# Kernel optimization log

Hardware: AMD Instinct MI355X
Metric: run time of the kernel (lower is better)

Reference implementation:

```python
import jax, jax.numpy as jnp
import numpy as np
from math import factorial as _f

E = 131072          # number of neighbour pairs (edges)
N_ATOMS = 8192
NUM_RADIAL = 16
L_BASIS = 3         # basis_max_degree -> 16 SH components
L_MOMENT = 4        # moment_max_degree -> 25 components
CUTOFF = 5.0

# ---------- Clebsch-Gordan coefficients (real spherical-harmonic basis) ----------

def _cg(j1, m1, j2, m2, j3, m3):
    if m1 + m2 != m3 or not (abs(j1 - j2) <= j3 <= j1 + j2):
        return 0.0
    pre = ((2 * j3 + 1) * _f(j3 + j1 - j2) * _f(j3 - j1 + j2) * _f(j1 + j2 - j3) / _f(j1 + j2 + j3 + 1)) ** 0.5
    pre *= (_f(j3 + m3) * _f(j3 - m3) * _f(j1 - m1) * _f(j1 + m1) * _f(j2 - m2) * _f(j2 + m2)) ** 0.5
    s = 0.0
    for k in range(max(0, j2 - j3 - m1, j1 - j3 + m2), min(j1 + j2 - j3, j1 - m1, j2 + m2) + 1):
        s += (-1.0) ** k / (_f(k) * _f(j1 + j2 - j3 - k) * _f(j1 - m1 - k) * _f(j2 + m2 - k) * _f(j3 - j2 + m1 + k) * _f(j3 - j1 - m2 + k))
    return pre * s

def _u(l):
    # complex -> real SH change of basis; rows index real m, cols complex m'
    U = np.zeros((2 * l + 1, 2 * l + 1), dtype=np.complex128)
    U[l, l] = 1.0
    s2 = 2.0 ** -0.5
    for m in range(1, l + 1):
        U[l + m, l + m] = (-1) ** m * s2
        U[l + m, l - m] = s2
        U[l - m, l - m] = 1j * s2
        U[l - m, l + m] = -1j * (-1) ** m * s2
    return U

def _real_cg(l1, l2, l3):
    C = np.zeros((2 * l1 + 1, 2 * l2 + 1, 2 * l3 + 1), dtype=np.complex128)
    for a in range(2 * l1 + 1):
        for b in range(2 * l2 + 1):
            for c in range(2 * l3 + 1):
                C[a, b, c] = _cg(l1, a - l1, l2, b - l2, l3, c - l3)
    M = np.einsum('ia,jb,kc,abc->ijk', _u(l1), _u(l2), _u(l3).conj(), C)
    R, I = M.real, M.imag  # coefficients are purely real or purely imaginary per path
    out = R if np.abs(R).sum() >= np.abs(I).sum() else I
    return out.astype(np.float32)

def _paths(lin, lout):
    return [(l1, l2, l3)
            for l1 in range(lin + 1) for l2 in range(lin + 1)
            for l3 in range(abs(l1 - l2), min(l1 + l2, lout) + 1)]

PATHS1 = _paths(L_BASIS, L_MOMENT)   # 40 paths
PATHS2 = _paths(L_MOMENT, L_MOMENT)  # 67 paths
CG1 = [jnp.asarray(_real_cg(*p)) for p in PATHS1]
CG2 = [jnp.asarray(_real_cg(*p)) for p in PATHS2]

# ---------- spherical harmonics up to l=3 (orthonormal real SH) ----------

def _sph_harm(u):
    x, y, z = u[:, 0], u[:, 1], u[:, 2]
    x2, y2, z2 = x * x, y * y, z * z
    sh = [
        jnp.full_like(x, 0.28209479177387814),
        0.4886025119029199 * y, 0.4886025119029199 * z, 0.4886025119029199 * x,
        1.0925484305920792 * x * y, 1.0925484305920792 * y * z,
        0.31539156525252005 * (3.0 * z2 - 1.0),
        1.0925484305920792 * x * z, 0.5462742152960396 * (x2 - y2),
        0.5900435899266435 * y * (3.0 * x2 - y2), 2.890611442640554 * x * y * z,
        0.4570457994644658 * y * (5.0 * z2 - 1.0), 0.3731763325901154 * z * (5.0 * z2 - 3.0),
        0.4570457994644658 * x * (5.0 * z2 - 1.0), 1.445305721320277 * z * (x2 - y2),
        0.5900435899266435 * x * (x2 - 3.0 * y2),
    ]
    return jnp.stack(sh, axis=-1)  # (E, 16)

def _basis(disp):
    r = jnp.linalg.norm(disp, axis=-1)                         # (E,)
    u = disp / jnp.maximum(r, 1e-9)[:, None]
    x = r / CUTOFF
    # sinc radial basis: sinc((k+1) * r / cutoff), k = 0..NUM_RADIAL-1
    rb = jnp.sinc(x[:, None] * jnp.arange(1, NUM_RADIAL + 1, dtype=disp.dtype))  # (E, K)
    # smooth (bump) cutoff, nan-safe under grad
    x2 = jnp.where(x < 1.0, x * x, 0.0)
    cut = jnp.where(x < 1.0, jnp.exp(1.0 - 1.0 / (1.0 - x2)), 0.0)
    sh = _sph_harm(u)                                          # (E, 16)
    return (cut[:, None] * sh)[:, :, None] * rb[:, None, :]    # (E, 16, K)

def _fused_tensor(y, w, paths, cgs):
    # y: (E, (Lin+1)^2, F); one learnable weight per CG path per feature
    dim_out = (L_MOMENT + 1) ** 2
    out = jnp.zeros((y.shape[0], dim_out, y.shape[-1]), dtype=y.dtype)
    for p, ((l1, l2, l3), C) in enumerate(zip(paths, cgs)):
        y1 = y[:, l1 * l1:(l1 + 1) ** 2, :]
        y2 = y[:, l2 * l2:(l2 + 1) ** 2, :]
        z = jnp.einsum('eif,ejf,ijk->ekf', y1, y2, C.astype(y.dtype))
        out = out.at[:, l3 * l3:(l3 + 1) ** 2, :].add(w[p] * z)
    return out


def setup_inputs() -> dict:
    key = jax.random.key(0)
    k1, k2, k3, k4, k5 = jax.random.split(key, 5)
    return {
        "atomic_numbers": jax.random.randint(k1, (N_ATOMS,), 0, 100, dtype=jnp.int32),
        "neighbour_displacements": jax.random.normal(k2, (E, 3), dtype=jnp.float32) * 2.0,
        "neighbour_indices": jax.random.randint(k3, (E, 2), 0, N_ATOMS),
        "tp_weights1": jax.random.normal(k4, (len(PATHS1), NUM_RADIAL), dtype=jnp.float32) * 0.2,
        "tp_weights2": jax.random.normal(k5, (len(PATHS2), NUM_RADIAL), dtype=jnp.float32) * 0.2,
    }


def reference(atomic_numbers, neighbour_displacements, neighbour_indices, tp_weights1, tp_weights2):
    y = _basis(neighbour_displacements)                 # (E, 16, F)
    y = _fused_tensor(y, tp_weights1, PATHS1, CG1)      # (E, 25, F)  moment 2
    y = _fused_tensor(y, tp_weights2, PATHS2, CG2)      # (E, 25, F)  moment 3
    return y
```

## Files before the change

kernel.cpp:

```cpp
#include <hip/hip_runtime.h>
#include <utility>

typedef unsigned int  u32;
typedef unsigned short u16;


struct CEnt { int i, j, k; double c; };
struct PathTab { int n; int s; CEnt e[400]; };
struct cxd { double re, im; };
struct URow { int n; int col[2]; cxd v[2]; };
struct MTab { double M[9][9][9]; };

constexpr double FT[14] = {1.,1.,2.,6.,24.,120.,720.,5040.,40320.,362880.,
                           3628800.,39916800.,479001600.,6227020800.};

constexpr double cabs_(double x){ return x < 0 ? -x : x; }

constexpr double csqrt_(double x){
  if (x <= 0.) return 0.;
  double g = 1.;
  while (g*g < x) g *= 2.;
  for (int it = 0; it < 50; ++it) g = 0.5*(g + x/g);
  return g;
}

constexpr double cg_(int j1,int m1,int j2,int m2,int j3,int m3){
  if (m1 + m2 != m3) return 0.;
  int dj = j1 - j2; if (dj < 0) dj = -dj;
  if (j3 < dj || j3 > j1 + j2) return 0.;
  double preA = (double)(2*j3+1)*FT[j3+j1-j2]*FT[j3-j1+j2]*FT[j1+j2-j3]/FT[j1+j2+j3+1];
  double preB = FT[j3+m3]*FT[j3-m3]*FT[j1-m1]*FT[j1+m1]*FT[j2-m2]*FT[j2+m2];
  double pre = csqrt_(preA)*csqrt_(preB);
  int kmin = 0;
  if (j2-j3-m1 > kmin) kmin = j2-j3-m1;
  if (j1-j3+m2 > kmin) kmin = j1-j3+m2;
  int kmax = j1+j2-j3;
  if (j1-m1 < kmax) kmax = j1-m1;
  if (j2+m2 < kmax) kmax = j2+m2;
  double s = 0.;
  for (int k = kmin; k <= kmax; ++k){
    double d = FT[k]*FT[j1+j2-j3-k]*FT[j1-m1-k]*FT[j2+m2-k]*FT[j3-j2+m1+k]*FT[j3-j1-m2+k];
    s += ((k & 1) ? -1.0 : 1.0)/d;
  }
  return pre*s;
}

constexpr URow urow_(int l, int r){
  URow R{};
  const double s2 = 0.7071067811865476;
  int m = r - l;
  if (m == 0){ R.n = 1; R.col[0] = l; R.v[0] = {1., 0.}; }
  else if (m > 0){
    R.n = 2;
    R.col[0] = l + m; R.v[0] = { (m & 1) ? -s2 : s2, 0. };
    R.col[1] = l - m; R.v[1] = { s2, 0. };
  } else {
    int mm = -m;
    R.n = 2;
    R.col[0] = l - mm; R.v[0] = { 0., s2 };
    R.col[1] = l + mm; R.v[1] = { 0., (mm & 1) ? s2 : -s2 };
  }
  return R;
}

constexpr cxd cmul_(cxd a, cxd b){ return { a.re*b.re - a.im*b.im, a.re*b.im + a.im*b.re }; }

constexpr MTab buildM(int l1, int l2, int l3){
  const int n1 = 2*l1+1, n2 = 2*l2+1, n3 = 2*l3+1;
  double cgd[9][9][9] = {};
  for (int a = 0; a < n1; ++a)
    for (int b = 0; b < n2; ++b)
      for (int c = 0; c < n3; ++c)
        cgd[a][b][c] = cg_(l1, a-l1, l2, b-l2, l3, c-l3);

  double MR[9][9][9] = {}; double MI[9][9][9] = {};
  double sR = 0., sI = 0.;
  for (int i = 0; i < n1; ++i){
    URow u1 = urow_(l1, i);
    for (int j = 0; j < n2; ++j){
      URow u2 = urow_(l2, j);
      for (int k = 0; k < n3; ++k){
        URow u3 = urow_(l3, k);
        double mre = 0., mim = 0.;
        for (int a = 0; a < u1.n; ++a)
          for (int b = 0; b < u2.n; ++b)
            for (int c = 0; c < u3.n; ++c){
              double cv = cgd[u1.col[a]][u2.col[b]][u3.col[c]];
              if (cv != 0.){
                cxd t = cmul_(u1.v[a], u2.v[b]);
                cxd u3c = { u3.v[c].re, -u3.v[c].im };
                t = cmul_(t, u3c);
                mre += t.re*cv; mim += t.im*cv;
              }
            }
        MR[i][j][k] = mre; MI[i][j][k] = mim;
        sR += cabs_(mre); sI += cabs_(mim);
      }
    }
  }
  const bool useR = (sR >= sI);
  MTab out{};
  for (int i = 0; i < n1; ++i)
    for (int j = 0; j < n2; ++j)
      for (int k = 0; k < n3; ++k)
        out.M[i][j][k] = useR ? MR[i][j][k] : MI[i][j][k];
  return out;
}

constexpr PathTab buildDiag(int l, int l3){
  MTab A = buildM(l, l, l3);
  PathTab P{}; P.n = 0; P.s = 1;
  const int n = 2*l+1, n3 = 2*l3+1;
  for (int i = 0; i < n; ++i)
    for (int j = i; j < n; ++j)
      for (int k = 0; k < n3; ++k){
        double v = A.M[i][j][k];
        if (j > i) v += A.M[j][i][k];
        if (cabs_(v) > 1e-12){
          if (P.n >= 400) { P.n = -1; return P; }
          P.e[P.n].i = i; P.e[P.n].j = j; P.e[P.n].k = k; P.e[P.n].c = v; P.n++;
        }
      }
  return P;
}

constexpr PathTab buildPair(int l1, int l2, int l3){
  MTab A = buildM(l1, l2, l3);
  MTab B = buildM(l2, l1, l3);
  const int n1 = 2*l1+1, n2 = 2*l2+1, n3 = 2*l3+1;
  bool okp = true, okm = true;
  for (int i = 0; i < n1; ++i)
    for (int j = 0; j < n2; ++j)
      for (int k = 0; k < n3; ++k){
        double a = A.M[i][j][k], b = B.M[j][i][k];
        if (cabs_(b - a) > 1e-9) okp = false;
        if (cabs_(b + a) > 1e-9) okm = false;
      }
  PathTab P{}; P.n = 0; P.s = okp ? 1 : (okm ? -1 : 0);
  if (P.s == 0) return P;
  for (int i = 0; i < n1; ++i)
    for (int j = 0; j < n2; ++j)
      for (int k = 0; k < n3; ++k){
        double v = A.M[i][j][k];
        if (cabs_(v) > 1e-12){
          if (P.n >= 400) { P.n = -1; return P; }
          P.e[P.n].i = i; P.e[P.n].j = j; P.e[P.n].k = k; P.e[P.n].c = v; P.n++;
        }
      }
  return P;
}

constexpr PathTab buildSingleTab(int l1, int l2, int l3){
  MTab A = buildM(l1, l2, l3);
  const int n1 = 2*l1+1, n2 = 2*l2+1, n3 = 2*l3+1;
  PathTab P{}; P.n = 0; P.s = 1;
  for (int i = 0; i < n1; ++i)
    for (int j = 0; j < n2; ++j)
      for (int k = 0; k < n3; ++k){
        double v = A.M[i][j][k];
        if (cabs_(v) > 1e-12){
          if (P.n >= 400) { P.n = -1; return P; }
          P.e[P.n].i = i; P.e[P.n].j = j; P.e[P.n].k = k; P.e[P.n].c = v; P.n++;
        }
      }
  return P;
}

template<int L,int L3>          struct TD_ { static constexpr PathTab t = buildDiag(L, L3); };
template<int L1,int L2,int L3>  struct TP_ { static constexpr PathTab t = buildPair(L1, L2, L3); };
template<int L1,int L2,int L3>  struct TS_ { static constexpr PathTab t = buildSingleTab(L1, L2, L3); };

constexpr int pidx(int lin, int lout, int a, int b, int c){
  int p = 0;
  for (int l1 = 0; l1 <= lin; ++l1)
    for (int l2 = 0; l2 <= lin; ++l2){
      int lo = l1 > l2 ? l1 - l2 : l2 - l1;
      int hi = (l1 + l2 < lout) ? l1 + l2 : lout;
      for (int l3 = lo; l3 <= hi; ++l3){
        if (l1 == a && l2 == b && l3 == c) return p;
        ++p;
      }
    }
  return -1;
}

#define G1LIST(X) \
  X(0, 0,0,0) X(1, 1,1,0) X(2, 1,1,1) X(3, 1,1,2) \
  X(4, 2,2,0) X(5, 2,2,1) X(6, 2,2,2) X(7, 2,2,3) X(8, 2,2,4) \
  X(9, 3,3,0) X(10,3,3,1) X(11,3,3,2) X(12,3,3,3) X(13,3,3,4) \
  X(14,0,1,1) X(15,0,2,2) X(16,0,3,3) \
  X(17,1,2,1) X(18,1,2,2) X(19,1,2,3) \
  X(20,1,3,2) X(21,1,3,3) X(22,1,3,4) \
  X(23,2,3,1) X(24,2,3,2) X(25,2,3,3) X(26,2,3,4)

struct Grp { int l1, l2, l3; };
#define G1ITEM(i,a,b,c) {a,b,c},
constexpr Grp G1A[27] = { G1LIST(G1ITEM) };
#undef G1ITEM

struct SlotTab { int base[28]; int s[27]; int total; };
constexpr SlotTab buildSlots(){
  SlotTab T{}; int b = 0;
  for (int i = 0; i < 27; ++i){
    int l1 = G1A[i].l1, l2 = G1A[i].l2, l3 = G1A[i].l3;
    int s = (l1 == l2) ? 1 : buildPair(l1, l2, l3).s;
    T.s[i] = s;
    T.base[i] = b;
    int w = 2*l3 + 1;
    b += (l1 != l2 && s == 0) ? 2*w : w;
  }
  T.base[27] = b; T.total = b;
  return T;
}
constexpr SlotTab ST1 = buildSlots();
constexpr int NS1v = ST1.total;


template<class TT,int L1,int L2,int BASE,int... S>
__device__ __forceinline__ void accS_(const float* __restrict__ y,
                                      float* __restrict__ o,
                                      std::integer_sequence<int, S...>){
  (( o[BASE + TT::t.e[S].k] +=
       (float)TT::t.e[S].c
       * (y[L1*L1 + TT::t.e[S].i] * y[L2*L2 + TT::t.e[S].j]) ), ...);
}
template<class TT,int L1,int L2,int BASE>
__device__ __forceinline__ void accS(const float* __restrict__ y,
                                     float* __restrict__ o){
  accS_<TT,L1,L2,BASE>(y, o, std::make_integer_sequence<int, TT::t.n>{});
}

template<int L3,int BASE,int... K>
__device__ __forceinline__ void zadds_(float* __restrict__ z,
                                       const float* __restrict__ Se, float w,
                                       std::integer_sequence<int, K...>){
  (( z[L3*L3 + K] = fmaf(w, Se[BASE + K], z[L3*L3 + K]) ), ...);
}
template<int L3,int BASE>
__device__ __forceinline__ void zadds(float* __restrict__ z,
                                      const float* __restrict__ Se, float w){
  zadds_<L3,BASE>(z, Se, w, std::make_integer_sequence<int, 2*L3+1>{});
}

template<class TT,int L1,int L2,int L3,int... S>
__device__ __forceinline__ void aps_(const float* __restrict__ y,
                                     float* __restrict__ o, float we,
                                     std::integer_sequence<int, S...>){
  (( o[L3*L3 + TT::t.e[S].k] +=
       (float)TT::t.e[S].c
       * (we * (y[L1*L1 + TT::t.e[S].i] * y[L2*L2 + TT::t.e[S].j])) ), ...);
}
template<class TT,int L1,int L2,int L3>
__device__ __forceinline__ void apply_tabs_(const float* __restrict__ y,
                                            float* __restrict__ o, float we){
  aps_<TT,L1,L2,L3>(y, o, we, std::make_integer_sequence<int, TT::t.n>{});
}

#define G2LIST(X) \
  X(0,0,0) X(1,1,0) X(1,1,1) X(1,1,2) \
  X(2,2,0) X(2,2,1) X(2,2,2) X(2,2,3) X(2,2,4) \
  X(3,3,0) X(3,3,1) X(3,3,2) X(3,3,3) X(3,3,4) \
  X(4,4,0) X(4,4,1) X(4,4,2) X(4,4,3) X(4,4,4) \
  X(0,1,1) X(0,2,2) X(0,3,3) X(0,4,4) \
  X(1,2,1) X(1,2,2) X(1,2,3) X(1,3,2) X(1,3,3) X(1,3,4) X(1,4,3) X(1,4,4) \
  X(2,3,1) X(2,3,2) X(2,3,3) X(2,3,4) X(2,4,2) X(2,4,3) X(2,4,4) \
  X(3,4,1) X(3,4,2) X(3,4,3) X(3,4,4)

static __device__ __forceinline__ void zbuild_s(float* __restrict__ z,
                                                const float* __restrict__ Se,
                                                const float* __restrict__ w1s,
                                                int f){
#define GB(gi,a,b,c) { \
    if constexpr (a == b) { \
      constexpr int pA_ = pidx(3,4,a,a,c); \
      zadds<c, ST1.base[gi]>(z, Se, w1s[pA_*16 + f]); \
    } else if constexpr (ST1.s[gi] != 0) { \
      constexpr int pA_ = pidx(3,4,a,b,c), pB_ = pidx(3,4,b,a,c); \
      const float we = fmaf((float)ST1.s[gi], w1s[pB_*16 + f], w1s[pA_*16 + f]); \
      zadds<c, ST1.base[gi]>(z, Se, we); \
    } else { \
      constexpr int pA_ = pidx(3,4,a,b,c), pB_ = pidx(3,4,b,a,c); \
      zadds<c, ST1.base[gi]>(z, Se, w1s[pA_*16 + f]); \
      zadds<c, ST1.base[gi] + 2*c + 1>(z, Se, w1s[pB_*16 + f]); \
    } }
  G1LIST(GB)
#undef GB
}

static __device__ __forceinline__ void stage2_s(const float* __restrict__ z,
                                                float* __restrict__ o,
                                                const float* __restrict__ w2s,
                                                int f){
#define G2(a,b,c) { \
    if constexpr (a == b) { \
      constexpr int p_ = pidx(4,4,a,a,c); \
      apply_tabs_<TD_<a,c>, a, b, c>(z, o, w2s[p_*16 + f]); \
    } else if constexpr (TP_<a,b,c>::t.s != 0) { \
      constexpr int pA_ = pidx(4,4,a,b,c), pB_ = pidx(4,4,b,a,c); \
      const float we = fmaf((float)TP_<a,b,c>::t.s, w2s[pB_*16 + f], w2s[pA_*16 + f]); \
      apply_tabs_<TP_<a,b,c>, a, b, c>(z, o, we); \
    } else { \
      constexpr int pA_ = pidx(4,4,a,b,c), pB_ = pidx(4,4,b,a,c); \
      apply_tabs_<TS_<a,b,c>, a, b, c>(z, o, w2s[pA_*16 + f]); \
      apply_tabs_<TS_<b,a,c>, b, a, c>(z, o, w2s[pB_*16 + f]); \
    } }
  G2LIST(G2)
#undef G2
}


__global__ __launch_bounds__(64) void acmd_kernelA(
    const float* __restrict__ disp,
    float* __restrict__ Sg, int E)
{
  __shared__ float tl[64 * NS1v];

  const int lt = threadIdx.x;
  const int e  = blockIdx.x*64 + lt;

  float Sout[NS1v];
#pragma unroll
  for (int k = 0; k < NS1v; ++k) Sout[k] = 0.f;

  if (e < E){
    const float dx = disp[3*e+0], dy = disp[3*e+1], dz = disp[3*e+2];
    const float r  = sqrtf(dx*dx + dy*dy + dz*dz);
    const float x  = r * (1.0f/5.0f);
    const float inv = 1.0f / fmaxf(r, 1e-9f);
    const float ux = dx*inv, uy = dy*inv, uz = dz*inv;
    const float cut = (x < 1.0f) ? expf(1.0f - 1.0f/(1.0f - x*x)) : 0.0f;

    const float sx2 = ux*ux, sy2 = uy*uy, sz2 = uz*uz;
    float s_[16];
    s_[0]  = 0.28209479177387814f;
    s_[1]  = 0.4886025119029199f*uy;
    s_[2]  = 0.4886025119029199f*uz;
    s_[3]  = 0.4886025119029199f*ux;
    s_[4]  = 1.0925484305920792f*ux*uy;
    s_[5]  = 1.0925484305920792f*uy*uz;
    s_[6]  = 0.31539156525252005f*(3.0f*sz2 - 1.0f);
    s_[7]  = 1.0925484305920792f*ux*uz;
    s_[8]  = 0.5462742152960396f*(sx2 - sy2);
    s_[9]  = 0.5900435899266435f*uy*(3.0f*sx2 - sy2);
    s_[10] = 2.890611442640554f*ux*uy*uz;
    s_[11] = 0.4570457994644658f*uy*(5.0f*sz2 - 1.0f);
    s_[12] = 0.3731763325901154f*uz*(5.0f*sz2 - 3.0f);
    s_[13] = 0.4570457994644658f*ux*(5.0f*sz2 - 1.0f);
    s_[14] = 1.445305721320277f*uz*(sx2 - sy2);
    s_[15] = 0.5900435899266435f*ux*(sx2 - 3.0f*sy2);
#pragma unroll
    for (int i = 0; i < 16; ++i) s_[i] *= cut;

#define GA(gi,a,b,c) { \
      if constexpr (a == b) accS<TD_<a,c>, a, b, ST1.base[gi]>(s_, Sout); \
      else if constexpr (ST1.s[gi] != 0) accS<TP_<a,b,c>, a, b, ST1.base[gi]>(s_, Sout); \
      else { accS<TS_<a,b,c>, a, b, ST1.base[gi]>(s_, Sout); \
             accS<TS_<b,a,c>, b, a, ST1.base[gi] + 2*c + 1>(s_, Sout); } }
    G1LIST(GA)
#undef GA
  }

#pragma unroll
  for (int k = 0; k < NS1v; ++k) tl[lt*NS1v + k] = Sout[k];
  __syncthreads();

  const long long base  = (long long)blockIdx.x * 64 * NS1v;
  const long long total = (long long)E * NS1v;
  for (int i = lt; i < 64*NS1v; i += 64){
    long long g = base + i;
    if (g < total) Sg[g] = tl[i];
  }
}


__global__ __launch_bounds__(256) void acmd_kernelC(
    const float* __restrict__ disp,
    const float* __restrict__ Sg,
    const float* __restrict__ w1g,
    const float* __restrict__ w2g,
    float* __restrict__ outf, int E)
{
  __shared__ float w1s[40*16];
  __shared__ float w2s[65*16];
  __shared__ float Ss[16 * NS1v];

  for (int i = threadIdx.x; i < 40*16; i += 256) w1s[i] = w1g[i];
  for (int i = threadIdx.x; i < 65*16; i += 256) w2s[i] = w2g[i];
  {
    const long long sbase = (long long)blockIdx.x * 16 * NS1v;
    const long long stot  = (long long)E * NS1v;
    for (int i = threadIdx.x; i < 16*NS1v; i += 256){
      long long g = sbase + i;
      Ss[i] = (g < stot) ? Sg[g] : 0.f;
    }
  }
  __syncthreads();

  const int le = threadIdx.x >> 4;
  const int f  = threadIdx.x & 15;
  const int e  = blockIdx.x*16 + le;
  if (e >= E) return;

  const float dx = disp[3*e+0], dy = disp[3*e+1], dz = disp[3*e+2];
  const float r  = sqrtf(dx*dx + dy*dy + dz*dz);
  const float x  = r * (1.0f/5.0f);
  const float tt = x * (float)(f + 1);
  const float pt = 3.14159265358979f * tt;
  const float rb = (pt > 1e-5f) ? (sinf(pt)/pt) : (1.0f - pt*pt*(1.0f/6.0f));
  const float rb2 = rb*rb;

  const float* Se = &Ss[le * NS1v];

  float z[25];
#pragma unroll
  for (int k = 0; k < 25; ++k) z[k] = 0.f;
  zbuild_s(z, Se, w1s, f);
#pragma unroll
  for (int k = 0; k < 25; ++k) z[k] *= rb2;

  float o[25];
#pragma unroll
  for (int k = 0; k < 25; ++k) o[k] = 0.f;
  stage2_s(z, o, w2s, f);

  float* dst = outf + (long long)e * 400;
#pragma unroll
  for (int k = 0; k < 25; ++k)
    dst[k*16 + f] = o[k];
}


extern "C" void kernel_launch(void* const* d_in, const int* in_sizes, int n_in,
                              void* d_out, int out_size, void* d_ws, size_t ws_size,
                              hipStream_t stream){
  const float* disp = (const float*)d_in[1];
  const float* w1   = (const float*)d_in[3];
  const float* w2   = (const float*)d_in[4];
  const int E = in_sizes[1] / 3;

  const size_t needS = (size_t)E * NS1v * sizeof(float);
  if (ws_size < needS) return;
  float* Sg = (float*)d_ws;

  const int blocksA = (E + 63) / 64;
  acmd_kernelA<<<blocksA, 64, 0, stream>>>(disp, Sg, E);

  const int blocksC = (E + 15) / 16;
  acmd_kernelC<<<blocksC, 256, 0, stream>>>(disp, Sg, w1, w2, (float*)d_out, E);
}
```

Baseline: 146.6 us.

## Transpose stage-1 workspace to slot-major, drop single-path tables, precombine weights

Stage-1 output is now stored slot-major (k*E+e), so kernel A writes coalesced directly from registers with 256-thread blocks and no shared-memory staging. Static asserts establish that every off-diagonal path pair is symmetric or antisymmetric, which removes the split single-path tables and shrinks the workspace slots. Kernel C precombines each pair of path weights into per-group weights in shared memory and pads the shared stage-1 tile stride to 136. The cost is strided gathers from the transposed workspace in kernel C and reliance on the symmetry assumption holding for all paths.

```diff
diff --git a/kernel.cpp b/kernel.cpp
--- a/kernel.cpp
+++ b/kernel.cpp
@@ -150,25 +150,8 @@
   return P;
 }
 
-constexpr PathTab buildSingleTab(int l1, int l2, int l3){
-  MTab A = buildM(l1, l2, l3);
-  const int n1 = 2*l1+1, n2 = 2*l2+1, n3 = 2*l3+1;
-  PathTab P{}; P.n = 0; P.s = 1;
-  for (int i = 0; i < n1; ++i)
-    for (int j = 0; j < n2; ++j)
-      for (int k = 0; k < n3; ++k){
-        double v = A.M[i][j][k];
-        if (cabs_(v) > 1e-12){
-          if (P.n >= 400) { P.n = -1; return P; }
-          P.e[P.n].i = i; P.e[P.n].j = j; P.e[P.n].k = k; P.e[P.n].c = v; P.n++;
-        }
-      }
-  return P;
-}
-
 template<int L,int L3>          struct TD_ { static constexpr PathTab t = buildDiag(L, L3); };
 template<int L1,int L2,int L3>  struct TP_ { static constexpr PathTab t = buildPair(L1, L2, L3); };
-template<int L1,int L2,int L3>  struct TS_ { static constexpr PathTab t = buildSingleTab(L1, L2, L3); };
 
 constexpr int pidx(int lin, int lout, int a, int b, int c){
   int p = 0;
@@ -193,6 +176,17 @@
   X(20,1,3,2) X(21,1,3,3) X(22,1,3,4) \
   X(23,2,3,1) X(24,2,3,2) X(25,2,3,3) X(26,2,3,4)
 
+#define G2LIST(X) \
+  X(0, 0,0,0) X(1, 1,1,0) X(2, 1,1,1) X(3, 1,1,2) \
+  X(4, 2,2,0) X(5, 2,2,1) X(6, 2,2,2) X(7, 2,2,3) X(8, 2,2,4) \
+  X(9, 3,3,0) X(10,3,3,1) X(11,3,3,2) X(12,3,3,3) X(13,3,3,4) \
+  X(14,4,4,0) X(15,4,4,1) X(16,4,4,2) X(17,4,4,3) X(18,4,4,4) \
+  X(19,0,1,1) X(20,0,2,2) X(21,0,3,3) X(22,0,4,4) \
+  X(23,1,2,1) X(24,1,2,2) X(25,1,2,3) X(26,1,3,2) X(27,1,3,3) X(28,1,3,4) \
+  X(29,1,4,3) X(30,1,4,4) \
+  X(31,2,3,1) X(32,2,3,2) X(33,2,3,3) X(34,2,3,4) X(35,2,4,2) X(36,2,4,3) X(37,2,4,4) \
+  X(38,3,4,1) X(39,3,4,2) X(40,3,4,3) X(41,3,4,4)
+
 struct Grp { int l1, l2, l3; };
 #define G1ITEM(i,a,b,c) {a,b,c},
 constexpr Grp G1A[27] = { G1LIST(G1ITEM) };
@@ -206,14 +200,30 @@
     int s = (l1 == l2) ? 1 : buildPair(l1, l2, l3).s;
     T.s[i] = s;
     T.base[i] = b;
-    int w = 2*l3 + 1;
-    b += (l1 != l2 && s == 0) ? 2*w : w;
+    b += 2*l3 + 1;
   }
   T.base[27] = b; T.total = b;
   return T;
 }
 constexpr SlotTab ST1 = buildSlots();
 constexpr int NS1v = ST1.total;
+static_assert(NS1v == 135, "stage-1 pair symmetry broken");
+#define G1CK(gi,a,b,c) && (a == b || ST1.s[gi] != 0)
+static_assert(true G1LIST(G1CK), "stage-1 pair not +-1");
+#undef G1CK
+#define G2CK(gi,a,b,c) && (a == b || buildPair(a,b,c).s != 0)
+static_assert(true G2LIST(G2CK), "stage-2 pair not +-1");
+#undef G2CK
+
+struct WCe { int pA, pB, s; };
+#define G1WC(gi,a,b,c) { pidx(3,4,a,b,c), pidx(3,4,b,a,c), (a==b) ? 0 : ST1.s[gi] },
+constexpr WCe WC1[27] = { G1LIST(G1WC) };
+#undef G1WC
+#define G2WC(gi,a,b,c) { pidx(4,4,a,b,c), pidx(4,4,b,a,c), (a==b) ? 0 : buildPair(a,b,c).s },
+constexpr WCe WC2[42] = { G2LIST(G2WC) };
+#undef G2WC
+
+#define SSTRIDE 136
 
 
 template<class TT,int L1,int L2,int BASE,int... S>
@@ -256,120 +266,75 @@
   aps_<TT,L1,L2,L3>(y, o, we, std::make_integer_sequence<int, TT::t.n>{});
 }
 
-#define G2LIST(X) \
-  X(0,0,0) X(1,1,0) X(1,1,1) X(1,1,2) \
-  X(2,2,0) X(2,2,1) X(2,2,2) X(2,2,3) X(2,2,4) \
-  X(3,3,0) X(3,3,1) X(3,3,2) X(3,3,3) X(3,3,4) \
-  X(4,4,0) X(4,4,1) X(4,4,2) X(4,4,3) X(4,4,4) \
-  X(0,1,1) X(0,2,2) X(0,3,3) X(0,4,4) \
-  X(1,2,1) X(1,2,2) X(1,2,3) X(1,3,2) X(1,3,3) X(1,3,4) X(1,4,3) X(1,4,4) \
-  X(2,3,1) X(2,3,2) X(2,3,3) X(2,3,4) X(2,4,2) X(2,4,3) X(2,4,4) \
-  X(3,4,1) X(3,4,2) X(3,4,3) X(3,4,4)
-
 static __device__ __forceinline__ void zbuild_s(float* __restrict__ z,
                                                 const float* __restrict__ Se,
-                                                const float* __restrict__ w1s,
+                                                const float* __restrict__ cw1,
                                                 int f){
-#define GB(gi,a,b,c) { \
-    if constexpr (a == b) { \
-      constexpr int pA_ = pidx(3,4,a,a,c); \
-      zadds<c, ST1.base[gi]>(z, Se, w1s[pA_*16 + f]); \
-    } else if constexpr (ST1.s[gi] != 0) { \
-      constexpr int pA_ = pidx(3,4,a,b,c), pB_ = pidx(3,4,b,a,c); \
-      const float we = fmaf((float)ST1.s[gi], w1s[pB_*16 + f], w1s[pA_*16 + f]); \
-      zadds<c, ST1.base[gi]>(z, Se, we); \
-    } else { \
-      constexpr int pA_ = pidx(3,4,a,b,c), pB_ = pidx(3,4,b,a,c); \
-      zadds<c, ST1.base[gi]>(z, Se, w1s[pA_*16 + f]); \
-      zadds<c, ST1.base[gi] + 2*c + 1>(z, Se, w1s[pB_*16 + f]); \
-    } }
+#define GB(gi,a,b,c) zadds<c, ST1.base[gi]>(z, Se, cw1[gi*16 + f]);
   G1LIST(GB)
 #undef GB
 }
 
 static __device__ __forceinline__ void stage2_s(const float* __restrict__ z,
                                                 float* __restrict__ o,
-                                                const float* __restrict__ w2s,
+                                                const float* __restrict__ cw2,
                                                 int f){
-#define G2(a,b,c) { \
-    if constexpr (a == b) { \
-      constexpr int p_ = pidx(4,4,a,a,c); \
-      apply_tabs_<TD_<a,c>, a, b, c>(z, o, w2s[p_*16 + f]); \
-    } else if constexpr (TP_<a,b,c>::t.s != 0) { \
-      constexpr int pA_ = pidx(4,4,a,b,c), pB_ = pidx(4,4,b,a,c); \
-      const float we = fmaf((float)TP_<a,b,c>::t.s, w2s[pB_*16 + f], w2s[pA_*16 + f]); \
-      apply_tabs_<TP_<a,b,c>, a, b, c>(z, o, we); \
-    } else { \
-      constexpr int pA_ = pidx(4,4,a,b,c), pB_ = pidx(4,4,b,a,c); \
-      apply_tabs_<TS_<a,b,c>, a, b, c>(z, o, w2s[pA_*16 + f]); \
-      apply_tabs_<TS_<b,a,c>, b, a, c>(z, o, w2s[pB_*16 + f]); \
-    } }
+#define G2(gi,a,b,c) { const float we = cw2[gi*16 + f]; \
+    if constexpr (a == b) apply_tabs_<TD_<a,c>, a, b, c>(z, o, we); \
+    else                  apply_tabs_<TP_<a,b,c>, a, b, c>(z, o, we); }
   G2LIST(G2)
 #undef G2
 }
 
 
-__global__ __launch_bounds__(64) void acmd_kernelA(
+__global__ __launch_bounds__(256) void acmd_kernelA(
     const float* __restrict__ disp,
     float* __restrict__ Sg, int E)
 {
-  __shared__ float tl[64 * NS1v];
-
-  const int lt = threadIdx.x;
-  const int e  = blockIdx.x*64 + lt;
+  const int e = blockIdx.x*256 + threadIdx.x;
+  if (e >= E) return;
+
+  const float dx = disp[3*e+0], dy = disp[3*e+1], dz = disp[3*e+2];
+  const float r  = sqrtf(dx*dx + dy*dy + dz*dz);
+  const float x  = r * (1.0f/5.0f);
+  const float inv = 1.0f / fmaxf(r, 1e-9f);
+  const float ux = dx*inv, uy = dy*inv, uz = dz*inv;
+  const float cut = (x < 1.0f) ? expf(1.0f - 1.0f/(1.0f - x*x)) : 0.0f;
+
+  const float sx2 = ux*ux, sy2 = uy*uy, sz2 = uz*uz;
+  float s_[16];
+  s_[0]  = 0.28209479177387814f;
+  s_[1]  = 0.4886025119029199f*uy;
+  s_[2]  = 0.4886025119029199f*uz;
+  s_[3]  = 0.4886025119029199f*ux;
+  s_[4]  = 1.0925484305920792f*ux*uy;
+  s_[5]  = 1.0925484305920792f*uy*uz;
+  s_[6]  = 0.31539156525252005f*(3.0f*sz2 - 1.0f);
+  s_[7]  = 1.0925484305920792f*ux*uz;
+  s_[8]  = 0.5462742152960396f*(sx2 - sy2);
+  s_[9]  = 0.5900435899266435f*uy*(3.0f*sx2 - sy2);
+  s_[10] = 2.890611442640554f*ux*uy*uz;
+  s_[11] = 0.4570457994644658f*uy*(5.0f*sz2 - 1.0f);
+  s_[12] = 0.3731763325901154f*uz*(5.0f*sz2 - 3.0f);
+  s_[13] = 0.4570457994644658f*ux*(5.0f*sz2 - 1.0f);
+  s_[14] = 1.445305721320277f*uz*(sx2 - sy2);
+  s_[15] = 0.5900435899266435f*ux*(sx2 - 3.0f*sy2);
+#pragma unroll
+  for (int i = 0; i < 16; ++i) s_[i] *= cut;
 
   float Sout[NS1v];
 #pragma unroll
   for (int k = 0; k < NS1v; ++k) Sout[k] = 0.f;
 
-  if (e < E){
-    const float dx = disp[3*e+0], dy = disp[3*e+1], dz = disp[3*e+2];
-    const float r  = sqrtf(dx*dx + dy*dy + dz*dz);
-    const float x  = r * (1.0f/5.0f);
-    const float inv = 1.0f / fmaxf(r, 1e-9f);
-    const float ux = dx*inv, uy = dy*inv, uz = dz*inv;
-    const float cut = (x < 1.0f) ? expf(1.0f - 1.0f/(1.0f - x*x)) : 0.0f;
-
-    const float sx2 = ux*ux, sy2 = uy*uy, sz2 = uz*uz;
-    float s_[16];
-    s_[0]  = 0.28209479177387814f;
-    s_[1]  = 0.4886025119029199f*uy;
-    s_[2]  = 0.4886025119029199f*uz;
-    s_[3]  = 0.4886025119029199f*ux;
-    s_[4]  = 1.0925484305920792f*ux*uy;
-    s_[5]  = 1.0925484305920792f*uy*uz;
-    s_[6]  = 0.31539156525252005f*(3.0f*sz2 - 1.0f);
-    s_[7]  = 1.0925484305920792f*ux*uz;
-    s_[8]  = 0.5462742152960396f*(sx2 - sy2);
-    s_[9]  = 0.5900435899266435f*uy*(3.0f*sx2 - sy2);
-    s_[10] = 2.890611442640554f*ux*uy*uz;
-    s_[11] = 0.4570457994644658f*uy*(5.0f*sz2 - 1.0f);
-    s_[12] = 0.3731763325901154f*uz*(5.0f*sz2 - 3.0f);
-    s_[13] = 0.4570457994644658f*ux*(5.0f*sz2 - 1.0f);
-    s_[14] = 1.445305721320277f*uz*(sx2 - sy2);
-    s_[15] = 0.5900435899266435f*ux*(sx2 - 3.0f*sy2);
-#pragma unroll
-    for (int i = 0; i < 16; ++i) s_[i] *= cut;
-
 #define GA(gi,a,b,c) { \
-      if constexpr (a == b) accS<TD_<a,c>, a, b, ST1.base[gi]>(s_, Sout); \
-      else if constexpr (ST1.s[gi] != 0) accS<TP_<a,b,c>, a, b, ST1.base[gi]>(s_, Sout); \
-      else { accS<TS_<a,b,c>, a, b, ST1.base[gi]>(s_, Sout); \
-             accS<TS_<b,a,c>, b, a, ST1.base[gi] + 2*c + 1>(s_, Sout); } }
-    G1LIST(GA)
+    if constexpr (a == b) accS<TD_<a,c>, a, b, ST1.base[gi]>(s_, Sout); \
+    else                  accS<TP_<a,b,c>, a, b, ST1.base[gi]>(s_, Sout); }
+  G1LIST(GA)
 #undef GA
-  }
-
-#pragma unroll
-  for (int k = 0; k < NS1v; ++k) tl[lt*NS1v + k] = Sout[k];
-  __syncthreads();
-
-  const long long base  = (long long)blockIdx.x * 64 * NS1v;
-  const long long total = (long long)E * NS1v;
-  for (int i = lt; i < 64*NS1v; i += 64){
-    long long g = base + i;
-    if (g < total) Sg[g] = tl[i];
-  }
+
+#pragma unroll
+  for (int k = 0; k < NS1v; ++k)
+    Sg[(long long)k*E + e] = Sout[k];
 }
 
 
@@ -380,18 +345,28 @@
     const float* __restrict__ w2g,
     float* __restrict__ outf, int E)
 {
-  __shared__ float w1s[40*16];
-  __shared__ float w2s[65*16];
-  __shared__ float Ss[16 * NS1v];
-
-  for (int i = threadIdx.x; i < 40*16; i += 256) w1s[i] = w1g[i];
-  for (int i = threadIdx.x; i < 65*16; i += 256) w2s[i] = w2g[i];
+  __shared__ float cw1s[27*16];
+  __shared__ float cw2s[42*16];
+  __shared__ __align__(16) float Ss[16 * SSTRIDE];
+
+  for (int i = threadIdx.x; i < 27*16; i += 256){
+    const int g = i >> 4, ff = i & 15;
+    float w = w1g[WC1[g].pA*16 + ff];
+    if (WC1[g].s) w = fmaf((float)WC1[g].s, w1g[WC1[g].pB*16 + ff], w);
+    cw1s[i] = w;
+  }
+  for (int i = threadIdx.x; i < 42*16; i += 256){
+    const int g = i >> 4, ff = i & 15;
+    float w = w2g[WC2[g].pA*16 + ff];
+    if (WC2[g].s) w = fmaf((float)WC2[g].s, w2g[WC2[g].pB*16 + ff], w);
+    cw2s[i] = w;
+  }
   {
-    const long long sbase = (long long)blockIdx.x * 16 * NS1v;
-    const long long stot  = (long long)E * NS1v;
+    const long long base = (long long)blockIdx.x * 16;
     for (int i = threadIdx.x; i < 16*NS1v; i += 256){
-      long long g = sbase + i;
-      Ss[i] = (g < stot) ? Sg[g] : 0.f;
+      const int slot = i >> 4, le = i & 15;
+      const long long ee = base + le;
+      Ss[le*SSTRIDE + slot] = (ee < E) ? Sg[(long long)slot*E + ee] : 0.f;
     }
   }
   __syncthreads();
@@ -409,19 +384,19 @@
   const float rb = (pt > 1e-5f) ? (sinf(pt)/pt) : (1.0f - pt*pt*(1.0f/6.0f));
   const float rb2 = rb*rb;
 
-  const float* Se = &Ss[le * NS1v];
+  const float* Se = &Ss[le * SSTRIDE];
 
   float z[25];
 #pragma unroll
   for (int k = 0; k < 25; ++k) z[k] = 0.f;
-  zbuild_s(z, Se, w1s, f);
+  zbuild_s(z, Se, cw1s, f);
 #pragma unroll
   for (int k = 0; k < 25; ++k) z[k] *= rb2;
 
   float o[25];
 #pragma unroll
   for (int k = 0; k < 25; ++k) o[k] = 0.f;
-  stage2_s(z, o, w2s, f);
+  stage2_s(z, o, cw2s, f);
 
   float* dst = outf + (long long)e * 400;
 #pragma unroll
@@ -442,8 +417,8 @@
   if (ws_size < needS) return;
   float* Sg = (float*)d_ws;
 
-  const int blocksA = (E + 63) / 64;
-  acmd_kernelA<<<blocksA, 64, 0, stream>>>(disp, Sg, E);
+  const int blocksA = (E + 255) / 256;
+  acmd_kernelA<<<blocksA, 256, 0, stream>>>(disp, Sg, E);
 
   const int blocksC = (E + 15) / 16;
   acmd_kernelC<<<blocksC, 256, 0, stream>>>(disp, Sg, w1, w2, (float*)d_out, E);
```

New measurement: 136.3 us. 1.08x faster.
